# Kernel optimization log

Hardware: AMD Instinct MI355X
Metric: run time of the kernel (lower is better)

The kernel has to match this reference:

```python
import jax, jax.numpy as jnp
import numpy as np

D_MODEL = 1024
NUM_HEADS = 16
D_K = D_MODEL // NUM_HEADS


def setup_inputs() -> dict:
    key = jax.random.key(0)
    ks = jax.random.split(key, 5)
    s = 1.0 / np.sqrt(D_MODEL)
    return {
        "x": jax.random.normal(ks[0], (2, 2048, D_MODEL), dtype=jnp.float32),
        "Wq": jax.random.normal(ks[1], (D_MODEL, D_MODEL), dtype=jnp.float32) * s,
        "bq": jnp.zeros((D_MODEL,), jnp.float32),
        "Wk": jax.random.normal(ks[2], (D_MODEL, D_MODEL), dtype=jnp.float32) * s,
        "bk": jnp.zeros((D_MODEL,), jnp.float32),
        "Wv": jax.random.normal(ks[3], (D_MODEL, D_MODEL), dtype=jnp.float32) * s,
        "bv": jnp.zeros((D_MODEL,), jnp.float32),
        "Wo": jax.random.normal(ks[4], (D_MODEL, D_MODEL), dtype=jnp.float32) * s,
        "bo": jnp.zeros((D_MODEL,), jnp.float32),
    }


def reference(x, Wq, bq, Wk, bk, Wv, bv, Wo, bo):
    B, S, _ = x.shape

    def split_heads(t):  # [B,S,D] -> [B,H,S,d_k]
        return t.reshape(B, S, NUM_HEADS, D_K).transpose(0, 2, 1, 3)

    q = split_heads(x @ Wq + bq)
    k = split_heads(x @ Wk + bk)
    v = split_heads(x @ Wv + bv)

    # [B,H,S,S] scores, scaled by 1/sqrt(d_k)
    scores = jnp.einsum("bhqd,bhkd->bhqk", q, k) / jnp.sqrt(jnp.float32(D_K))
    causal = jnp.tril(jnp.ones((S, S), dtype=bool))  # True = keep
    scores = jnp.where(causal, scores, -jnp.inf)
    attn = jax.nn.softmax(scores, axis=-1)
    # dropout is identity in eval mode
    out = jnp.einsum("bhqk,bhkd->bhqd", attn, v)
    out = out.transpose(0, 2, 1, 3).reshape(B, S, D_MODEL)
    return out @ Wo + bo
```

## Files before the change

kernel.cpp:

```cpp
#include <hip/hip_runtime.h>
#include <stdint.h>

typedef __attribute__((ext_vector_type(8))) short bf16x8;
typedef __attribute__((ext_vector_type(8))) unsigned short ushort8;
typedef __attribute__((ext_vector_type(4))) float f32x4;
typedef __attribute__((ext_vector_type(16))) float f32x16;

constexpr int DM = 1024;
constexpr int SQ = 2048;
constexpr int NB = 2;
constexpr int NH = 16;
constexpr int DK = 64;
constexpr int M  = NB * SQ;

__device__ inline float bf2f(unsigned short u) {
    union { uint32_t i; float f; } c; c.i = ((uint32_t)u) << 16; return c.f;
}
__device__ inline unsigned short f2bf(float f) {
    union { float f; uint32_t i; } c; c.f = f;
    uint32_t r = c.i + 0x7FFFu + ((c.i >> 16) & 1u);
    return (unsigned short)(r >> 16);
}
__device__ inline float exp2v(float x) {
    float r;
    asm("v_exp_f32 %0, %1" : "=v"(r) : "v"(x));
    return r;
}
__device__ inline uint32_t cvtpk(float lo, float hi) {
    uint32_t r;
    asm("v_cvt_pk_bf16_f32 %0, %1, %2" : "=v"(r) : "v"(lo), "v"(hi));
    return r;
}
__device__ inline uint32_t sx32(uint32_t v) {
    return (uint32_t)__shfl_xor((int)v, 32);
}
__device__ inline bf16x8 mkfrag(uint32_t a, uint32_t b, uint32_t c, uint32_t d) {
    union { bf16x8 v; uint32_t u[4]; } m;
    m.u[0] = a; m.u[1] = b; m.u[2] = c; m.u[3] = d;
    return m.v;
}
__device__ inline void gload_lds16(const unsigned short* g, unsigned short* l) {
    __builtin_amdgcn_global_load_lds(
        (const __attribute__((address_space(1))) void*)g,
        (__attribute__((address_space(3))) void*)l, 16, 0, 0);
}

__global__ __launch_bounds__(256) void cvt_x(const float* __restrict__ x,
                                             unsigned short* __restrict__ xb) {
    int idx = (blockIdx.x * 256 + threadIdx.x) * 8;
    const float* p = x + idx;
    ushort8 o;
#pragma unroll
    for (int i = 0; i < 8; ++i) o[i] = f2bf(p[i]);
    *(ushort8*)(xb + idx) = o;
}

__global__ __launch_bounds__(256) void cvt_w(const float* __restrict__ W,
                                             unsigned short* __restrict__ Wt) {
    __shared__ float tile[32][33];
    int tx = threadIdx.x, ty = threadIdx.y;
    int bx = blockIdx.x, by = blockIdx.y;
#pragma unroll
    for (int j = 0; j < 4; ++j)
        tile[ty + j * 8][tx] = W[(size_t)(by * 32 + ty + j * 8) * DM + bx * 32 + tx];
    __syncthreads();
#pragma unroll
    for (int j = 0; j < 4; ++j)
        Wt[(size_t)(bx * 32 + ty + j * 8) * DM + by * 32 + tx] = f2bf(tile[tx][ty + j * 8]);
}

template <int MODE>
__global__ __launch_bounds__(256) void gemm128(const unsigned short* __restrict__ A,
                                               const unsigned short* __restrict__ Bt,
                                               const float* __restrict__ b0,
                                               const float* __restrict__ b1,
                                               const float* __restrict__ b2,
                                               void* __restrict__ outp) {
    constexpr int K = 1024;
    __shared__ __align__(16) unsigned short As[128 * 32];
    __shared__ __align__(16) unsigned short Bs[128 * 32];
    const int t = threadIdx.x;
    const int w = t >> 6, l = t & 63;
    const int l15 = l & 15, lg = l >> 4;
    const int wr = w >> 1, wc = w & 1;
    const int bx = blockIdx.x, by = blockIdx.y;

    f32x4 acc[4][4] = {};

    const int srow = l >> 2;
    const int sk   = (l & 3) * 8;
    const unsigned short* Abase = A  + (size_t)(by * 128) * K;
    const unsigned short* Bbase = Bt + (size_t)(bx * 128) * K;

    for (int k0 = 0; k0 < K; k0 += 32) {
#pragma unroll
        for (int i = 0; i < 2; ++i) {
            const int row = w * 32 + i * 16 + srow;
            gload_lds16(Abase + (size_t)row * K + k0 + sk, &As[row * 32 + sk]);
            gload_lds16(Bbase + (size_t)row * K + k0 + sk, &Bs[row * 32 + sk]);
        }
        __syncthreads();

        bf16x8 af[4], bfr[4];
#pragma unroll
        for (int mi = 0; mi < 4; ++mi)
            af[mi] = *(const bf16x8*)&As[(wr * 64 + mi * 16 + l15) * 32 + lg * 8];
#pragma unroll
        for (int ni = 0; ni < 4; ++ni)
            bfr[ni] = *(const bf16x8*)&Bs[(wc * 64 + ni * 16 + l15) * 32 + lg * 8];
#pragma unroll
        for (int mi = 0; mi < 4; ++mi)
#pragma unroll
            for (int ni = 0; ni < 4; ++ni)
                acc[mi][ni] = __builtin_amdgcn_mfma_f32_16x16x32_bf16(af[mi], bfr[ni], acc[mi][ni], 0, 0, 0);
        __syncthreads();
    }

#pragma unroll
    for (int ni = 0; ni < 4; ++ni) {
        const int n = bx * 128 + wc * 64 + ni * 16 + l15;
        float bias;
        if constexpr (MODE == 0) {
            const int mat = n >> 10;
            const float* bp = (mat == 0) ? b0 : (mat == 1) ? b1 : b2;
            bias = bp[n & 1023];
        } else {
            bias = b0[n];
        }
#pragma unroll
        for (int mi = 0; mi < 4; ++mi)
#pragma unroll
            for (int i = 0; i < 4; ++i) {
                const int m = by * 128 + wr * 64 + mi * 16 + lg * 4 + i;
                float v = acc[mi][ni][i] + bias;
                if constexpr (MODE == 0) {
                    const int mat = n >> 10, c = n & 1023;
                    if (mat == 0) v *= 0.18033688f;
                    const int h = c >> 6, d = c & 63;
                    const int b = m >> 11, si = m & 2047;
                    size_t idx;
                    if (mat == 2)
                        idx = ((size_t)(b * NH + h) * DK + d) * SQ + si;
                    else
                        idx = ((size_t)(b * NH + h) * SQ + si) * DK + d;
                    ((unsigned short*)outp)[(size_t)mat * (NB * NH * SQ * DK) + idx] = f2bf(v);
                } else {
                    ((float*)outp)[(size_t)m * DM + n] = v;
                }
            }
    }
}

__global__ __launch_bounds__(128) void attn32(const unsigned short* __restrict__ Qg,
                                              const unsigned short* __restrict__ Kg,
                                              const unsigned short* __restrict__ Vtg,
                                              unsigned short* __restrict__ O) {
    __shared__ __align__(16) char KV[2][16384];
    const float NEG_INF = -__builtin_inff();

    const int bid = blockIdx.x;
    const int bh  = bid & 31;
    const int pr  = bid >> 5;
    const int b = bh >> 4, h = bh & 15;
    const size_t base = (size_t)bh * SQ * DK;

    const int t = threadIdx.x;
    const int w = t >> 6, l = t & 63;
    const int l31 = l & 31, hi = l >> 5;
    const bool h0 = (hi == 0);

    char* Ks0 = KV[w];
    char* Vs0 = KV[w] + 8192;
    float* myP = (float*)KV[w];
    float* otP = (float*)KV[w ^ 1];

    const int lrow = l >> 3;
    const int lchunk = (l & 7) ^ lrow;
    const unsigned short* ksrc0 = Kg + base + (size_t)lrow * DK + lchunk * 8;
    const unsigned short* vsrc0 = Vtg + (size_t)(bh * 64 + lrow) * SQ + lchunk * 8;

    int roff[4];
#pragma unroll
    for (int c = 0; c < 4; ++c) roff[c] = (hi * 16 + 32 * c) ^ ((l & 7) << 4);
    const int rb0 = l31 * 128, rb1 = (32 + l31) * 128;

#pragma unroll 1
    for (int half = 0; half < 2; ++half) {
        const int qi   = half ? (63 - pr) : pr;
        const int T    = (qi >> 1) + 1;
        const int Tmax = (T + 1) >> 1;
        const int qrow = qi * 32 + l31;

        bf16x8 qf[4];
        {
            const unsigned short* qp = Qg + base + (size_t)qrow * DK + hi * 8;
#pragma unroll
            for (int c = 0; c < 4; ++c) qf[c] = *(const bf16x8*)(qp + 16 * c);
        }

        float mrun = NEG_INF, lsum = 0.f;
        f32x16 o0 = {}, o1 = {};

#pragma unroll 1
        for (int i = 0; i < Tmax; ++i) {
            const int kt = 2 * i + w;
            const bool act = kt < T;
            if (act) {
                const unsigned short* ks = ksrc0 + (size_t)kt * 64 * DK;
                const unsigned short* vs = vsrc0 + kt * 64;
#pragma unroll
                for (int j = 0; j < 8; ++j)
                    gload_lds16(ks + j * 8 * DK, (unsigned short*)Ks0 + j * 512 + l * 8);
#pragma unroll
                for (int j = 0; j < 8; ++j)
                    gload_lds16(vs + (size_t)j * 8 * SQ, (unsigned short*)Vs0 + j * 512 + l * 8);
            }
            __syncthreads();
            if (!act) continue;

            f32x16 s0v = {}, s1v = {};
#pragma unroll
            for (int c = 0; c < 4; ++c) {
                bf16x8 ka0 = *(const bf16x8*)(Ks0 + rb0 + roff[c]);
                bf16x8 ka1 = *(const bf16x8*)(Ks0 + rb1 + roff[c]);
                s0v = __builtin_amdgcn_mfma_f32_32x32x16_bf16(ka0, qf[c], s0v, 0, 0, 0);
                s1v = __builtin_amdgcn_mfma_f32_32x32x16_bf16(ka1, qf[c], s1v, 0, 0, 0);
            }

            float s[32];
#pragma unroll
            for (int r = 0; r < 16; ++r) { s[r] = s0v[r]; s[16 + r] = s1v[r]; }
            if (kt == T - 1) {
                const int qrel = qrow - kt * 64;
#pragma unroll
                for (int r = 0; r < 16; ++r) {
                    const int key0 = (r & 3) + 8 * (r >> 2) + 4 * hi;
                    if (key0 > qrel) s[r] = NEG_INF;
                    if (key0 + 32 > qrel) s[16 + r] = NEG_INF;
                }
            }

            float t8[8];
#pragma unroll
            for (int j = 0; j < 8; ++j)
                t8[j] = fmaxf(fmaxf(s[j], s[j + 8]), fmaxf(s[j + 16], s[j + 24]));
            float tm = fmaxf(fmaxf(fmaxf(t8[0], t8[1]), fmaxf(t8[2], t8[3])),
                             fmaxf(fmaxf(t8[4], t8[5]), fmaxf(t8[6], t8[7])));
            tm = fmaxf(tm, __shfl_xor(tm, 32));

            const float mn = fmaxf(mrun, tm);
            if (!__all(tm - mrun <= 11.0f)) {
                const float corr = exp2v(mrun - mn);
                lsum *= corr;
#pragma unroll
                for (int r = 0; r < 16; ++r) { o0[r] *= corr; o1[r] *= corr; }
                mrun = mn;
            }

#pragma unroll
            for (int r = 0; r < 32; ++r) s[r] = exp2v(s[r] - mrun);
            float a8[8];
#pragma unroll
            for (int j = 0; j < 8; ++j)
                a8[j] = (s[j] + s[j + 8]) + (s[j + 16] + s[j + 24]);
            lsum += ((a8[0] + a8[1]) + (a8[2] + a8[3])) + ((a8[4] + a8[5]) + (a8[6] + a8[7]));

            uint32_t pk[16];
#pragma unroll
            for (int j = 0; j < 16; ++j) pk[j] = cvtpk(s[2 * j], s[2 * j + 1]);
            const uint32_t X1 = sx32(h0 ? pk[2]  : pk[0]);
            const uint32_t X2 = sx32(h0 ? pk[3]  : pk[1]);
            const uint32_t X3 = sx32(h0 ? pk[6]  : pk[4]);
            const uint32_t X4 = sx32(h0 ? pk[7]  : pk[5]);
            const uint32_t X5 = sx32(h0 ? pk[10] : pk[8]);
            const uint32_t X6 = sx32(h0 ? pk[11] : pk[9]);
            const uint32_t X7 = sx32(h0 ? pk[14] : pk[12]);
            const uint32_t X8 = sx32(h0 ? pk[15] : pk[13]);
            bf16x8 pf[4];
            pf[0] = mkfrag(h0 ? pk[0]  : X1, h0 ? pk[1]  : X2, h0 ? X1 : pk[2],  h0 ? X2 : pk[3]);
            pf[1] = mkfrag(h0 ? pk[4]  : X3, h0 ? pk[5]  : X4, h0 ? X3 : pk[6],  h0 ? X4 : pk[7]);
            pf[2] = mkfrag(h0 ? pk[8]  : X5, h0 ? pk[9]  : X6, h0 ? X5 : pk[10], h0 ? X6 : pk[11]);
            pf[3] = mkfrag(h0 ? pk[12] : X7, h0 ? pk[13] : X8, h0 ? X7 : pk[14], h0 ? X8 : pk[15]);

#pragma unroll
            for (int vi = 0; vi < 4; ++vi) {
                bf16x8 va0 = *(const bf16x8*)(Vs0 + rb0 + roff[vi]);
                bf16x8 va1 = *(const bf16x8*)(Vs0 + rb1 + roff[vi]);
                o0 = __builtin_amdgcn_mfma_f32_32x32x16_bf16(va0, pf[vi], o0, 0, 0, 0);
                o1 = __builtin_amdgcn_mfma_f32_32x32x16_bf16(va1, pf[vi], o1, 0, 0, 0);
            }
        }

        lsum += __shfl_xor(lsum, 32);
        {
            float* pb = myP + (size_t)l * 40;
#pragma unroll
            for (int r = 0; r < 16; ++r) { pb[r] = o0[r]; pb[16 + r] = o1[r]; }
            pb[32] = mrun; pb[33] = lsum;
        }
        __syncthreads();
        float lm;
        {
            const float* qb = otP + (size_t)l * 40;
            const float pm = qb[32], pl = qb[33];
            const float mm = fmaxf(mrun, pm);
            const float ca = exp2v(mrun - mm);
            const float cb = exp2v(pm - mm);
            lm = lsum * ca + pl * cb;
#pragma unroll
            for (int r = 0; r < 16; ++r) {
                o0[r] = o0[r] * ca + qb[r] * cb;
                o1[r] = o1[r] * ca + qb[16 + r] * cb;
            }
        }
        __syncthreads();

        if (w == half) {
            const float inv = 1.f / lm;
            unsigned short* op = O + ((size_t)(b * SQ + qrow)) * DM + h * 64;
#pragma unroll
            for (int r = 0; r < 16; r += 2) {
                const int d = (r & 3) + 8 * (r >> 2) + 4 * hi;
                uint32_t w0 = (uint32_t)f2bf(o0[r] * inv) | ((uint32_t)f2bf(o0[r + 1] * inv) << 16);
                uint32_t w1 = (uint32_t)f2bf(o1[r] * inv) | ((uint32_t)f2bf(o1[r + 1] * inv) << 16);
                *(uint32_t*)(op + d) = w0;
                *(uint32_t*)(op + 32 + d) = w1;
            }
        }
    }
}

extern "C" void kernel_launch(void* const* d_in, const int* in_sizes, int n_in,
                              void* d_out, int out_size, void* d_ws, size_t ws_size,
                              hipStream_t stream) {
    const float* x  = (const float*)d_in[0];
    const float* Wq = (const float*)d_in[1];
    const float* bq = (const float*)d_in[2];
    const float* Wk = (const float*)d_in[3];
    const float* bk = (const float*)d_in[4];
    const float* Wv = (const float*)d_in[5];
    const float* bv = (const float*)d_in[6];
    const float* Wo = (const float*)d_in[7];
    const float* bo = (const float*)d_in[8];
    float* out = (float*)d_out;

    char* ws = (char*)d_ws;
    const size_t XB_BYTES = (size_t)M * DM * 2;
    const size_t W_BYTES  = (size_t)DM * DM * 2;
    const size_t H_BYTES  = (size_t)NB * NH * SQ * DK * 2;
    unsigned short* xb  = (unsigned short*)ws;
    unsigned short* wqt = (unsigned short*)(ws + XB_BYTES);
    unsigned short* wkt = (unsigned short*)(ws + XB_BYTES + W_BYTES);
    unsigned short* wvt = (unsigned short*)(ws + XB_BYTES + 2 * W_BYTES);
    unsigned short* wot = (unsigned short*)(ws + XB_BYTES + 3 * W_BYTES);
    unsigned short* Qb  = (unsigned short*)(ws + XB_BYTES + 4 * W_BYTES);
    unsigned short* Kb  = (unsigned short*)(ws + XB_BYTES + 4 * W_BYTES + H_BYTES);
    unsigned short* Vb  = (unsigned short*)(ws + XB_BYTES + 4 * W_BYTES + 2 * H_BYTES);

    cvt_x<<<(M * DM) / (256 * 8), 256, 0, stream>>>(x, xb);
    dim3 wgrid(32, 32), wblk(32, 8);
    cvt_w<<<wgrid, wblk, 0, stream>>>(Wq, wqt);
    cvt_w<<<wgrid, wblk, 0, stream>>>(Wk, wkt);
    cvt_w<<<wgrid, wblk, 0, stream>>>(Wv, wvt);
    cvt_w<<<wgrid, wblk, 0, stream>>>(Wo, wot);

    gemm128<0><<<dim3(24, 32), 256, 0, stream>>>(xb, wqt, bq, bk, bv, Qb);

    attn32<<<NB * NH * 32, 128, 0, stream>>>(Qb, Kb, Vb, xb );

    gemm128<1><<<dim3(8, 32), 256, 0, stream>>>(xb, wot, bo, bo, bo, out);
}
```

Before: 129.2 us.

## Split attention KV loop across four waves with direct global loads; merge weight casts

The attention kernel now runs four waves per block instead of two. Each wave takes every fourth KV tile and reads K and V fragments straight from global memory, where before they were staged through LDS with async loads and a barrier per iteration. Waves 1-3 write their partial softmax state to LDS and wave 0 merges all of them and writes the output. The four weight conversion launches are fused into one 3D-grid launch. This removes the per-tile barriers and adds parallelism, at the cost of uncoalesced, uncached global fragment loads and a serial merge step in wave 0.

```diff
diff --git a/kernel.cpp b/kernel.cpp
--- a/kernel.cpp
+++ b/kernel.cpp
@@ -55,9 +55,15 @@
     *(ushort8*)(xb + idx) = o;
 }
 
-__global__ __launch_bounds__(256) void cvt_w(const float* __restrict__ W,
-                                             unsigned short* __restrict__ Wt) {
+__global__ __launch_bounds__(256) void cvt_w4(const float* __restrict__ W0,
+                                              const float* __restrict__ W1,
+                                              const float* __restrict__ W2,
+                                              const float* __restrict__ W3,
+                                              unsigned short* __restrict__ WtBase) {
     __shared__ float tile[32][33];
+    const int z = blockIdx.z;
+    const float* W = (z == 0) ? W0 : (z == 1) ? W1 : (z == 2) ? W2 : W3;
+    unsigned short* Wt = WtBase + (size_t)z * DM * DM;
     int tx = threadIdx.x, ty = threadIdx.y;
     int bx = blockIdx.x, by = blockIdx.y;
 #pragma unroll
@@ -151,11 +157,11 @@
     }
 }
 
-__global__ __launch_bounds__(128) void attn32(const unsigned short* __restrict__ Qg,
-                                              const unsigned short* __restrict__ Kg,
-                                              const unsigned short* __restrict__ Vtg,
-                                              unsigned short* __restrict__ O) {
-    __shared__ __align__(16) char KV[2][16384];
+__global__ __launch_bounds__(256, 4) void attn32(const unsigned short* __restrict__ Qg,
+                                                 const unsigned short* __restrict__ Kg,
+                                                 const unsigned short* __restrict__ Vtg,
+                                                 unsigned short* __restrict__ O) {
+    __shared__ float Pl[3][64 * 35];
     const float NEG_INF = -__builtin_inff();
 
     const int bid = blockIdx.x;
@@ -169,26 +175,13 @@
     const int l31 = l & 31, hi = l >> 5;
     const bool h0 = (hi == 0);
 
-    char* Ks0 = KV[w];
-    char* Vs0 = KV[w] + 8192;
-    float* myP = (float*)KV[w];
-    float* otP = (float*)KV[w ^ 1];
-
-    const int lrow = l >> 3;
-    const int lchunk = (l & 7) ^ lrow;
-    const unsigned short* ksrc0 = Kg + base + (size_t)lrow * DK + lchunk * 8;
-    const unsigned short* vsrc0 = Vtg + (size_t)(bh * 64 + lrow) * SQ + lchunk * 8;
-
-    int roff[4];
-#pragma unroll
-    for (int c = 0; c < 4; ++c) roff[c] = (hi * 16 + 32 * c) ^ ((l & 7) << 4);
-    const int rb0 = l31 * 128, rb1 = (32 + l31) * 128;
+    const unsigned short* krow0 = Kg + base + (size_t)l31 * DK + hi * 8;
+    const unsigned short* vrow0 = Vtg + (size_t)(bh * 64 + l31) * SQ + hi * 8;
 
 #pragma unroll 1
     for (int half = 0; half < 2; ++half) {
         const int qi   = half ? (63 - pr) : pr;
         const int T    = (qi >> 1) + 1;
-        const int Tmax = (T + 1) >> 1;
         const int qrow = qi * 32 + l31;
 
         bf16x8 qf[4];
@@ -202,27 +195,13 @@
         f32x16 o0 = {}, o1 = {};
 
 #pragma unroll 1
-        for (int i = 0; i < Tmax; ++i) {
-            const int kt = 2 * i + w;
-            const bool act = kt < T;
-            if (act) {
-                const unsigned short* ks = ksrc0 + (size_t)kt * 64 * DK;
-                const unsigned short* vs = vsrc0 + kt * 64;
-#pragma unroll
-                for (int j = 0; j < 8; ++j)
-                    gload_lds16(ks + j * 8 * DK, (unsigned short*)Ks0 + j * 512 + l * 8);
-#pragma unroll
-                for (int j = 0; j < 8; ++j)
-                    gload_lds16(vs + (size_t)j * 8 * SQ, (unsigned short*)Vs0 + j * 512 + l * 8);
-            }
-            __syncthreads();
-            if (!act) continue;
-
+        for (int kt = w; kt < T; kt += 4) {
+            const unsigned short* kp = krow0 + (size_t)kt * 64 * DK;
             f32x16 s0v = {}, s1v = {};
 #pragma unroll
             for (int c = 0; c < 4; ++c) {
-                bf16x8 ka0 = *(const bf16x8*)(Ks0 + rb0 + roff[c]);
-                bf16x8 ka1 = *(const bf16x8*)(Ks0 + rb1 + roff[c]);
+                bf16x8 ka0 = *(const bf16x8*)(kp + 16 * c);
+                bf16x8 ka1 = *(const bf16x8*)(kp + (size_t)32 * DK + 16 * c);
                 s0v = __builtin_amdgcn_mfma_f32_32x32x16_bf16(ka0, qf[c], s0v, 0, 0, 0);
                 s1v = __builtin_amdgcn_mfma_f32_32x32x16_bf16(ka1, qf[c], s1v, 0, 0, 0);
             }
@@ -282,41 +261,42 @@
             pf[2] = mkfrag(h0 ? pk[8]  : X5, h0 ? pk[9]  : X6, h0 ? X5 : pk[10], h0 ? X6 : pk[11]);
             pf[3] = mkfrag(h0 ? pk[12] : X7, h0 ? pk[13] : X8, h0 ? X7 : pk[14], h0 ? X8 : pk[15]);
 
+            const unsigned short* vp = vrow0 + kt * 64;
 #pragma unroll
             for (int vi = 0; vi < 4; ++vi) {
-                bf16x8 va0 = *(const bf16x8*)(Vs0 + rb0 + roff[vi]);
-                bf16x8 va1 = *(const bf16x8*)(Vs0 + rb1 + roff[vi]);
+                bf16x8 va0 = *(const bf16x8*)(vp + 16 * vi);
+                bf16x8 va1 = *(const bf16x8*)(vp + (size_t)32 * SQ + 16 * vi);
                 o0 = __builtin_amdgcn_mfma_f32_32x32x16_bf16(va0, pf[vi], o0, 0, 0, 0);
                 o1 = __builtin_amdgcn_mfma_f32_32x32x16_bf16(va1, pf[vi], o1, 0, 0, 0);
             }
         }
 
         lsum += __shfl_xor(lsum, 32);
-        {
-            float* pb = myP + (size_t)l * 40;
+
+        if (w) {
+            float* pb = Pl[w - 1] + (size_t)l * 35;
 #pragma unroll
             for (int r = 0; r < 16; ++r) { pb[r] = o0[r]; pb[16 + r] = o1[r]; }
             pb[32] = mrun; pb[33] = lsum;
         }
         __syncthreads();
-        float lm;
-        {
-            const float* qb = otP + (size_t)l * 40;
-            const float pm = qb[32], pl = qb[33];
-            const float mm = fmaxf(mrun, pm);
-            const float ca = exp2v(mrun - mm);
-            const float cb = exp2v(pm - mm);
-            lm = lsum * ca + pl * cb;
-#pragma unroll
-            for (int r = 0; r < 16; ++r) {
-                o0[r] = o0[r] * ca + qb[r] * cb;
-                o1[r] = o1[r] * ca + qb[16 + r] * cb;
-            }
-        }
-        __syncthreads();
-
-        if (w == half) {
-            const float inv = 1.f / lm;
+        if (w == 0) {
+#pragma unroll 1
+            for (int j = 0; j < 3; ++j) {
+                const float* qb = Pl[j] + (size_t)l * 35;
+                const float pm = qb[32], pl = qb[33];
+                const float mm = fmaxf(mrun, pm);
+                const float ca = exp2v(mrun - mm);
+                const float cb = exp2v(pm - mm);
+                lsum = lsum * ca + pl * cb;
+#pragma unroll
+                for (int r = 0; r < 16; ++r) {
+                    o0[r] = o0[r] * ca + qb[r] * cb;
+                    o1[r] = o1[r] * ca + qb[16 + r] * cb;
+                }
+                mrun = mm;
+            }
+            const float inv = 1.f / lsum;
             unsigned short* op = O + ((size_t)(b * SQ + qrow)) * DM + h * 64;
 #pragma unroll
             for (int r = 0; r < 16; r += 2) {
@@ -327,6 +307,7 @@
                 *(uint32_t*)(op + 32 + d) = w1;
             }
         }
+        __syncthreads();
     }
 }
 
@@ -350,23 +331,17 @@
     const size_t H_BYTES  = (size_t)NB * NH * SQ * DK * 2;
     unsigned short* xb  = (unsigned short*)ws;
     unsigned short* wqt = (unsigned short*)(ws + XB_BYTES);
-    unsigned short* wkt = (unsigned short*)(ws + XB_BYTES + W_BYTES);
-    unsigned short* wvt = (unsigned short*)(ws + XB_BYTES + 2 * W_BYTES);
     unsigned short* wot = (unsigned short*)(ws + XB_BYTES + 3 * W_BYTES);
     unsigned short* Qb  = (unsigned short*)(ws + XB_BYTES + 4 * W_BYTES);
     unsigned short* Kb  = (unsigned short*)(ws + XB_BYTES + 4 * W_BYTES + H_BYTES);
     unsigned short* Vb  = (unsigned short*)(ws + XB_BYTES + 4 * W_BYTES + 2 * H_BYTES);
 
     cvt_x<<<(M * DM) / (256 * 8), 256, 0, stream>>>(x, xb);
-    dim3 wgrid(32, 32), wblk(32, 8);
-    cvt_w<<<wgrid, wblk, 0, stream>>>(Wq, wqt);
-    cvt_w<<<wgrid, wblk, 0, stream>>>(Wk, wkt);
-    cvt_w<<<wgrid, wblk, 0, stream>>>(Wv, wvt);
-    cvt_w<<<wgrid, wblk, 0, stream>>>(Wo, wot);
+    cvt_w4<<<dim3(32, 32, 4), dim3(32, 8), 0, stream>>>(Wq, Wk, Wv, Wo, wqt);
 
     gemm128<0><<<dim3(24, 32), 256, 0, stream>>>(xb, wqt, bq, bk, bv, Qb);
 
-    attn32<<<NB * NH * 32, 128, 0, stream>>>(Qb, Kb, Vb, xb );
+    attn32<<<NB * NH * 32, 256, 0, stream>>>(Qb, Kb, Vb, xb );
 
     gemm128<1><<<dim3(8, 32), 256, 0, stream>>>(xb, wot, bo, bo, bo, out);
 }
```

Result: slower. 154.8 us (+19.8%).

## Launch one attention block per query tile and fuse weight conversion launches

Applied to the files above, without the earlier changes.

The attention kernel previously paired a light and a heavy causal query tile per block and looped over both. It now launches one block per 32-row query tile (2048 blocks), heaviest tiles first, and merges the two waves' partial results directly into the output store. The four weight-conversion launches are folded into one launch using a z grid dimension. This is meant to raise parallelism and cut launch overhead, at the cost of less balanced per-block work and more blocks overall.

```diff
diff --git a/kernel.cpp b/kernel.cpp
--- a/kernel.cpp
+++ b/kernel.cpp
@@ -34,6 +34,9 @@
 __device__ inline uint32_t sx32(uint32_t v) {
     return (uint32_t)__shfl_xor((int)v, 32);
 }
+__device__ inline float sx32f(float v) {
+    return __shfl_xor(v, 32);
+}
 __device__ inline bf16x8 mkfrag(uint32_t a, uint32_t b, uint32_t c, uint32_t d) {
     union { bf16x8 v; uint32_t u[4]; } m;
     m.u[0] = a; m.u[1] = b; m.u[2] = c; m.u[3] = d;
@@ -55,9 +58,15 @@
     *(ushort8*)(xb + idx) = o;
 }
 
-__global__ __launch_bounds__(256) void cvt_w(const float* __restrict__ W,
-                                             unsigned short* __restrict__ Wt) {
+__global__ __launch_bounds__(256) void cvt_w4(const float* __restrict__ W0,
+                                              const float* __restrict__ W1,
+                                              const float* __restrict__ W2,
+                                              const float* __restrict__ W3,
+                                              unsigned short* __restrict__ WtBase) {
     __shared__ float tile[32][33];
+    const int z = blockIdx.z;
+    const float* W = (z == 0) ? W0 : (z == 1) ? W1 : (z == 2) ? W2 : W3;
+    unsigned short* Wt = WtBase + (size_t)z * DM * DM;
     int tx = threadIdx.x, ty = threadIdx.y;
     int bx = blockIdx.x, by = blockIdx.y;
 #pragma unroll
@@ -160,7 +169,7 @@
 
     const int bid = blockIdx.x;
     const int bh  = bid & 31;
-    const int pr  = bid >> 5;
+    const int qi  = 63 - (bid >> 5);
     const int b = bh >> 4, h = bh & 15;
     const size_t base = (size_t)bh * SQ * DK;
 
@@ -184,145 +193,137 @@
     for (int c = 0; c < 4; ++c) roff[c] = (hi * 16 + 32 * c) ^ ((l & 7) << 4);
     const int rb0 = l31 * 128, rb1 = (32 + l31) * 128;
 
+    const int T    = (qi >> 1) + 1;
+    const int Tmax = (T + 1) >> 1;
+    const int qrow = qi * 32 + l31;
+
+    bf16x8 qf[4];
+    {
+        const unsigned short* qp = Qg + base + (size_t)qrow * DK + hi * 8;
+#pragma unroll
+        for (int c = 0; c < 4; ++c) qf[c] = *(const bf16x8*)(qp + 16 * c);
+    }
+
+    float mrun = NEG_INF, lsum = 0.f;
+    f32x16 o0 = {}, o1 = {};
+
 #pragma unroll 1
-    for (int half = 0; half < 2; ++half) {
-        const int qi   = half ? (63 - pr) : pr;
-        const int T    = (qi >> 1) + 1;
-        const int Tmax = (T + 1) >> 1;
-        const int qrow = qi * 32 + l31;
-
-        bf16x8 qf[4];
-        {
-            const unsigned short* qp = Qg + base + (size_t)qrow * DK + hi * 8;
-#pragma unroll
-            for (int c = 0; c < 4; ++c) qf[c] = *(const bf16x8*)(qp + 16 * c);
-        }
-
-        float mrun = NEG_INF, lsum = 0.f;
-        f32x16 o0 = {}, o1 = {};
-
-#pragma unroll 1
-        for (int i = 0; i < Tmax; ++i) {
-            const int kt = 2 * i + w;
-            const bool act = kt < T;
-            if (act) {
-                const unsigned short* ks = ksrc0 + (size_t)kt * 64 * DK;
-                const unsigned short* vs = vsrc0 + kt * 64;
-#pragma unroll
-                for (int j = 0; j < 8; ++j)
-                    gload_lds16(ks + j * 8 * DK, (unsigned short*)Ks0 + j * 512 + l * 8);
-#pragma unroll
-                for (int j = 0; j < 8; ++j)
-                    gload_lds16(vs + (size_t)j * 8 * SQ, (unsigned short*)Vs0 + j * 512 + l * 8);
+    for (int i = 0; i < Tmax; ++i) {
+        const int kt = 2 * i + w;
+        const bool act = kt < T;
+        if (act) {
+            const unsigned short* ks = ksrc0 + (size_t)kt * 64 * DK;
+            const unsigned short* vs = vsrc0 + kt * 64;
+#pragma unroll
+            for (int j = 0; j < 8; ++j)
+                gload_lds16(ks + j * 8 * DK, (unsigned short*)Ks0 + j * 512 + l * 8);
+#pragma unroll
+            for (int j = 0; j < 8; ++j)
+                gload_lds16(vs + (size_t)j * 8 * SQ, (unsigned short*)Vs0 + j * 512 + l * 8);
+        }
+        __syncthreads();
+        if (!act) continue;
+
+        f32x16 s0v = {}, s1v = {};
+#pragma unroll
+        for (int c = 0; c < 4; ++c) {
+            bf16x8 ka0 = *(const bf16x8*)(Ks0 + rb0 + roff[c]);
+            bf16x8 ka1 = *(const bf16x8*)(Ks0 + rb1 + roff[c]);
+            s0v = __builtin_amdgcn_mfma_f32_32x32x16_bf16(ka0, qf[c], s0v, 0, 0, 0);
+            s1v = __builtin_amdgcn_mfma_f32_32x32x16_bf16(ka1, qf[c], s1v, 0, 0, 0);
+        }
+
+        float s[32];
+#pragma unroll
+        for (int r = 0; r < 16; ++r) { s[r] = s0v[r]; s[16 + r] = s1v[r]; }
+        if (kt == T - 1) {
+            const int qrel = qrow - kt * 64;
+#pragma unroll
+            for (int r = 0; r < 16; ++r) {
+                const int key0 = (r & 3) + 8 * (r >> 2) + 4 * hi;
+                if (key0 > qrel) s[r] = NEG_INF;
+                if (key0 + 32 > qrel) s[16 + r] = NEG_INF;
             }
-            __syncthreads();
-            if (!act) continue;
-
-            f32x16 s0v = {}, s1v = {};
-#pragma unroll
-            for (int c = 0; c < 4; ++c) {
-                bf16x8 ka0 = *(const bf16x8*)(Ks0 + rb0 + roff[c]);
-                bf16x8 ka1 = *(const bf16x8*)(Ks0 + rb1 + roff[c]);
-                s0v = __builtin_amdgcn_mfma_f32_32x32x16_bf16(ka0, qf[c], s0v, 0, 0, 0);
-                s1v = __builtin_amdgcn_mfma_f32_32x32x16_bf16(ka1, qf[c], s1v, 0, 0, 0);
-            }
-
-            float s[32];
-#pragma unroll
-            for (int r = 0; r < 16; ++r) { s[r] = s0v[r]; s[16 + r] = s1v[r]; }
-            if (kt == T - 1) {
-                const int qrel = qrow - kt * 64;
-#pragma unroll
-                for (int r = 0; r < 16; ++r) {
-                    const int key0 = (r & 3) + 8 * (r >> 2) + 4 * hi;
-                    if (key0 > qrel) s[r] = NEG_INF;
-                    if (key0 + 32 > qrel) s[16 + r] = NEG_INF;
-                }
-            }
-
-            float t8[8];
-#pragma unroll
-            for (int j = 0; j < 8; ++j)
-                t8[j] = fmaxf(fmaxf(s[j], s[j + 8]), fmaxf(s[j + 16], s[j + 24]));
-            float tm = fmaxf(fmaxf(fmaxf(t8[0], t8[1]), fmaxf(t8[2], t8[3])),
-                             fmaxf(fmaxf(t8[4], t8[5]), fmaxf(t8[6], t8[7])));
-            tm = fmaxf(tm, __shfl_xor(tm, 32));
-
-            const float mn = fmaxf(mrun, tm);
-            if (!__all(tm - mrun <= 11.0f)) {
-                const float corr = exp2v(mrun - mn);
-                lsum *= corr;
-#pragma unroll
-                for (int r = 0; r < 16; ++r) { o0[r] *= corr; o1[r] *= corr; }
-                mrun = mn;
-            }
-
-#pragma unroll
-            for (int r = 0; r < 32; ++r) s[r] = exp2v(s[r] - mrun);
-            float a8[8];
-#pragma unroll
-            for (int j = 0; j < 8; ++j)
-                a8[j] = (s[j] + s[j + 8]) + (s[j + 16] + s[j + 24]);
-            lsum += ((a8[0] + a8[1]) + (a8[2] + a8[3])) + ((a8[4] + a8[5]) + (a8[6] + a8[7]));
-
-            uint32_t pk[16];
-#pragma unroll
-            for (int j = 0; j < 16; ++j) pk[j] = cvtpk(s[2 * j], s[2 * j + 1]);
-            const uint32_t X1 = sx32(h0 ? pk[2]  : pk[0]);
-            const uint32_t X2 = sx32(h0 ? pk[3]  : pk[1]);
-            const uint32_t X3 = sx32(h0 ? pk[6]  : pk[4]);
-            const uint32_t X4 = sx32(h0 ? pk[7]  : pk[5]);
-            const uint32_t X5 = sx32(h0 ? pk[10] : pk[8]);
-            const uint32_t X6 = sx32(h0 ? pk[11] : pk[9]);
-            const uint32_t X7 = sx32(h0 ? pk[14] : pk[12]);
-            const uint32_t X8 = sx32(h0 ? pk[15] : pk[13]);
-            bf16x8 pf[4];
-            pf[0] = mkfrag(h0 ? pk[0]  : X1, h0 ? pk[1]  : X2, h0 ? X1 : pk[2],  h0 ? X2 : pk[3]);
-            pf[1] = mkfrag(h0 ? pk[4]  : X3, h0 ? pk[5]  : X4, h0 ? X3 : pk[6],  h0 ? X4 : pk[7]);
-            pf[2] = mkfrag(h0 ? pk[8]  : X5, h0 ? pk[9]  : X6, h0 ? X5 : pk[10], h0 ? X6 : pk[11]);
-            pf[3] = mkfrag(h0 ? pk[12] : X7, h0 ? pk[13] : X8, h0 ? X7 : pk[14], h0 ? X8 : pk[15]);
-
-#pragma unroll
-            for (int vi = 0; vi < 4; ++vi) {
-                bf16x8 va0 = *(const bf16x8*)(Vs0 + rb0 + roff[vi]);
-                bf16x8 va1 = *(const bf16x8*)(Vs0 + rb1 + roff[vi]);
-                o0 = __builtin_amdgcn_mfma_f32_32x32x16_bf16(va0, pf[vi], o0, 0, 0, 0);
-                o1 = __builtin_amdgcn_mfma_f32_32x32x16_bf16(va1, pf[vi], o1, 0, 0, 0);
-            }
-        }
-
-        lsum += __shfl_xor(lsum, 32);
-        {
-            float* pb = myP + (size_t)l * 40;
-#pragma unroll
-            for (int r = 0; r < 16; ++r) { pb[r] = o0[r]; pb[16 + r] = o1[r]; }
-            pb[32] = mrun; pb[33] = lsum;
-        }
-        __syncthreads();
-        float lm;
-        {
-            const float* qb = otP + (size_t)l * 40;
-            const float pm = qb[32], pl = qb[33];
-            const float mm = fmaxf(mrun, pm);
-            const float ca = exp2v(mrun - mm);
-            const float cb = exp2v(pm - mm);
-            lm = lsum * ca + pl * cb;
-#pragma unroll
-            for (int r = 0; r < 16; ++r) {
-                o0[r] = o0[r] * ca + qb[r] * cb;
-                o1[r] = o1[r] * ca + qb[16 + r] * cb;
-            }
-        }
-        __syncthreads();
-
-        if (w == half) {
+        }
+
+        float t8[8];
+#pragma unroll
+        for (int j = 0; j < 8; ++j)
+            t8[j] = fmaxf(fmaxf(s[j], s[j + 8]), fmaxf(s[j + 16], s[j + 24]));
+        float tm = fmaxf(fmaxf(fmaxf(t8[0], t8[1]), fmaxf(t8[2], t8[3])),
+                         fmaxf(fmaxf(t8[4], t8[5]), fmaxf(t8[6], t8[7])));
+        tm = fmaxf(tm, sx32f(tm));
+
+        const float mn = fmaxf(mrun, tm);
+        if (!__all(tm - mrun <= 11.0f)) {
+            const float corr = exp2v(mrun - mn);
+            lsum *= corr;
+#pragma unroll
+            for (int r = 0; r < 16; ++r) { o0[r] *= corr; o1[r] *= corr; }
+            mrun = mn;
+        }
+
+#pragma unroll
+        for (int r = 0; r < 32; ++r) s[r] = exp2v(s[r] - mrun);
+        float a8[8];
+#pragma unroll
+        for (int j = 0; j < 8; ++j)
+            a8[j] = (s[j] + s[j + 8]) + (s[j + 16] + s[j + 24]);
+        lsum += ((a8[0] + a8[1]) + (a8[2] + a8[3])) + ((a8[4] + a8[5]) + (a8[6] + a8[7]));
+
+        uint32_t pk[16];
+#pragma unroll
+        for (int j = 0; j < 16; ++j) pk[j] = cvtpk(s[2 * j], s[2 * j + 1]);
+        const uint32_t X1 = sx32(h0 ? pk[2]  : pk[0]);
+        const uint32_t X2 = sx32(h0 ? pk[3]  : pk[1]);
+        const uint32_t X3 = sx32(h0 ? pk[6]  : pk[4]);
+        const uint32_t X4 = sx32(h0 ? pk[7]  : pk[5]);
+        const uint32_t X5 = sx32(h0 ? pk[10] : pk[8]);
+        const uint32_t X6 = sx32(h0 ? pk[11] : pk[9]);
+        const uint32_t X7 = sx32(h0 ? pk[14] : pk[12]);
+        const uint32_t X8 = sx32(h0 ? pk[15] : pk[13]);
+        bf16x8 pf[4];
+        pf[0] = mkfrag(h0 ? pk[0]  : X1, h0 ? pk[1]  : X2, h0 ? X1 : pk[2],  h0 ? X2 : pk[3]);
+        pf[1] = mkfrag(h0 ? pk[4]  : X3, h0 ? pk[5]  : X4, h0 ? X3 : pk[6],  h0 ? X4 : pk[7]);
+        pf[2] = mkfrag(h0 ? pk[8]  : X5, h0 ? pk[9]  : X6, h0 ? X5 : pk[10], h0 ? X6 : pk[11]);
+        pf[3] = mkfrag(h0 ? pk[12] : X7, h0 ? pk[13] : X8, h0 ? X7 : pk[14], h0 ? X8 : pk[15]);
+
+#pragma unroll
+        for (int vi = 0; vi < 4; ++vi) {
+            bf16x8 va0 = *(const bf16x8*)(Vs0 + rb0 + roff[vi]);
+            bf16x8 va1 = *(const bf16x8*)(Vs0 + rb1 + roff[vi]);
+            o0 = __builtin_amdgcn_mfma_f32_32x32x16_bf16(va0, pf[vi], o0, 0, 0, 0);
+            o1 = __builtin_amdgcn_mfma_f32_32x32x16_bf16(va1, pf[vi], o1, 0, 0, 0);
+        }
+    }
+
+    lsum += sx32f(lsum);
+    {
+        float* pb = myP + (size_t)l * 40;
+#pragma unroll
+        for (int r = 0; r < 16; ++r) { pb[r] = o0[r]; pb[16 + r] = o1[r]; }
+        pb[32] = mrun; pb[33] = lsum;
+    }
+    __syncthreads();
+    {
+        const float* qb = otP + (size_t)l * 40;
+        const float pm = qb[32], pl = qb[33];
+        const float mm = fmaxf(mrun, pm);
+        const float ca = exp2v(mrun - mm);
+        const float cb = exp2v(pm - mm);
+        const float lm = lsum * ca + pl * cb;
+        if (w == 0) {
             const float inv = 1.f / lm;
             unsigned short* op = O + ((size_t)(b * SQ + qrow)) * DM + h * 64;
 #pragma unroll
             for (int r = 0; r < 16; r += 2) {
                 const int d = (r & 3) + 8 * (r >> 2) + 4 * hi;
-                uint32_t w0 = (uint32_t)f2bf(o0[r] * inv) | ((uint32_t)f2bf(o0[r + 1] * inv) << 16);
-                uint32_t w1 = (uint32_t)f2bf(o1[r] * inv) | ((uint32_t)f2bf(o1[r + 1] * inv) << 16);
+                const float e0 = o0[r] * ca + qb[r] * cb;
+                const float e1 = o0[r + 1] * ca + qb[r + 1] * cb;
+                const float f0 = o1[r] * ca + qb[16 + r] * cb;
+                const float f1 = o1[r + 1] * ca + qb[16 + r + 1] * cb;
+                uint32_t w0 = (uint32_t)f2bf(e0 * inv) | ((uint32_t)f2bf(e1 * inv) << 16);
+                uint32_t w1 = (uint32_t)f2bf(f0 * inv) | ((uint32_t)f2bf(f1 * inv) << 16);
                 *(uint32_t*)(op + d) = w0;
                 *(uint32_t*)(op + 32 + d) = w1;
             }
@@ -350,23 +351,17 @@
     const size_t H_BYTES  = (size_t)NB * NH * SQ * DK * 2;
     unsigned short* xb  = (unsigned short*)ws;
     unsigned short* wqt = (unsigned short*)(ws + XB_BYTES);
-    unsigned short* wkt = (unsigned short*)(ws + XB_BYTES + W_BYTES);
-    unsigned short* wvt = (unsigned short*)(ws + XB_BYTES + 2 * W_BYTES);
     unsigned short* wot = (unsigned short*)(ws + XB_BYTES + 3 * W_BYTES);
     unsigned short* Qb  = (unsigned short*)(ws + XB_BYTES + 4 * W_BYTES);
     unsigned short* Kb  = (unsigned short*)(ws + XB_BYTES + 4 * W_BYTES + H_BYTES);
     unsigned short* Vb  = (unsigned short*)(ws + XB_BYTES + 4 * W_BYTES + 2 * H_BYTES);
 
     cvt_x<<<(M * DM) / (256 * 8), 256, 0, stream>>>(x, xb);
-    dim3 wgrid(32, 32), wblk(32, 8);
-    cvt_w<<<wgrid, wblk, 0, stream>>>(Wq, wqt);
-    cvt_w<<<wgrid, wblk, 0, stream>>>(Wk, wkt);
-    cvt_w<<<wgrid, wblk, 0, stream>>>(Wv, wvt);
-    cvt_w<<<wgrid, wblk, 0, stream>>>(Wo, wot);
+    cvt_w4<<<dim3(32, 32, 4), dim3(32, 8), 0, stream>>>(Wq, Wk, Wv, Wo, wqt);
 
     gemm128<0><<<dim3(24, 32), 256, 0, stream>>>(xb, wqt, bq, bk, bv, Qb);
 
-    attn32<<<NB * NH * 32, 128, 0, stream>>>(Qb, Kb, Vb, xb );
+    attn32<<<NB * NH * 64, 128, 0, stream>>>(Qb, Kb, Vb, xb );
 
     gemm128<1><<<dim3(8, 32), 256, 0, stream>>>(xb, wot, bo, bo, bo, out);
 }
```

Measured after the change: 122.7 us. 5.0% less time.
